# Kernel optimization log

Hardware: AMD Instinct MI355X
Metric: run time of the kernel (lower is better)

## Reference

```python
import jax, jax.numpy as jnp
import numpy as np

T, N, D, R, E = 512, 32, 300, 3, 64
NUM_NODES, VG = 70000, 40000


def setup_inputs() -> dict:
    key = jax.random.key(0)
    ks = jax.random.split(key, 10)
    return {
        "x_indices": jax.random.randint(ks[0], (T, N), 0, NUM_NODES),
        "edge_src": jax.random.randint(ks[1], (T, R, E), 0, N),
        "edge_dst": jax.random.randint(ks[2], (T, R, E), 0, N),
        "X": jax.random.normal(ks[3], (NUM_NODES, D), dtype=jnp.float32) * 0.1,
        "conv_W": jax.random.normal(ks[4], (R, D, D), dtype=jnp.float32) * 0.05,
        "W0": jax.random.normal(ks[5], (D, D), dtype=jnp.float32) * 0.05,
        "Wu": jax.random.normal(ks[6], (N * D, D), dtype=jnp.float32) * 0.01,
        "Uu": jax.random.normal(ks[7], (D, D), dtype=jnp.float32) * 0.05,
        "Wg": jax.random.normal(ks[8], (VG, D), dtype=jnp.float32) * 0.05,
        "bg": jnp.zeros((VG,), dtype=jnp.float32),
    }


def gcn_conv(x, W, src, dst):
    """torch_geometric GCNConv(bias=False): add self-loops, D^-1/2 (A+I) D^-1/2 (x W)."""
    n = x.shape[0]
    h = x @ W  # [N, D]
    loop = jnp.arange(n)
    s = jnp.concatenate([src, loop])
    t = jnp.concatenate([dst, loop])
    deg = jax.ops.segment_sum(jnp.ones_like(t, dtype=x.dtype), t, num_segments=n)
    dinv = jnp.where(deg > 0, jax.lax.rsqrt(jnp.maximum(deg, 1e-12)), 0.0)
    norm = dinv[s] * dinv[t]  # [E+N]
    return jax.ops.segment_sum(h[s] * norm[:, None], t, num_segments=n)


def reference(x_indices, edge_src, edge_dst, X, conv_W, W0, Wu, Uu, Wg, bg):
    def step(mem, inp):
        idx, src, dst = inp  # [N], [R,E], [R,E]
        x = X[idx]  # grapharea features [N, D]
        # sum of per-relation GCNConv outputs
        conv = jnp.sum(
            jax.vmap(gcn_conv, in_axes=(None, 0, 0, 0))(x, conv_W, src, dst), axis=0
        )
        proposed = conv + x @ W0  # eye(N) @ (x @ W0) == x @ W0
        # GRU-style update gate: [1, N*D] @ [N*D, D] + mem_row0 @ [D, D]
        gate = jax.nn.sigmoid(x.reshape(1, -1) @ Wu + mem[0:1] @ Uu)  # [1, D]
        new_mem = gate * proposed + (1.0 - gate) * mem  # broadcast over N rows
        logits = jnp.maximum(new_mem[0], 0.0) @ Wg.T + bg  # [VG]
        # memory is a non-grad buffer in torch (.data.copy_): stop gradient through time
        return jax.lax.stop_gradient(new_mem), jax.nn.log_softmax(logits)

    mem0 = jnp.zeros((N, D), dtype=X.dtype)
    _, log_probs = jax.lax.scan(step, mem0, (x_indices, edge_src, edge_dst))
    # include_senses=False: per-step torch.tensor(0) stacked -> zeros([T])
    return log_probs, jnp.zeros((x_indices.shape[0],), dtype=jnp.int32)
```

## Files before the change

kernel.cpp:

```cpp
#include <hip/hip_runtime.h>
#include <hip/hip_bf16.h>
#include <math.h>

#define T_ 512
#define N_ 32
#define D_ 300
#define R_ 3
#define E_ 64
#define VG_ 40000

typedef __attribute__((ext_vector_type(8))) short bf16x8;
typedef __attribute__((ext_vector_type(4))) float f32x4;

#define LGKM_BARRIER() asm volatile("s_waitcnt lgkmcnt(0)\n\ts_barrier" ::: "memory")

static __device__ inline unsigned short f2b(float f) {
  __hip_bfloat16 h = __float2bfloat16(f);
  return *(unsigned short*)&h;
}

__global__ void k_zero(float* __restrict__ p, int n) {
  int i = blockIdx.x * blockDim.x + threadIdx.x;
  if (i < n) p[i] = 0.f;
}

__global__ void k_tr_wu(const float* __restrict__ Wu, unsigned short* __restrict__ Wt) {
  __shared__ float s[32][33];
  int kb = blockIdx.x * 32, nb = blockIdx.y * 32;
  int tn = threadIdx.x & 31, tr = threadIdx.x >> 5;
  for (int i = tr; i < 32; i += 8) {
    int k = kb + i, n = nb + tn;
    s[i][tn] = (n < 300) ? Wu[(size_t)k * 300 + n] : 0.f;
  }
  __syncthreads();
  for (int i = tr; i < 32; i += 8) {
    int n = nb + i, k = kb + tn;
    Wt[(size_t)n * 9600 + k] = f2b(s[tn][i]);
  }
}

__global__ void k_tr_wcat(const float* __restrict__ convW, const float* __restrict__ W0,
                          unsigned short* __restrict__ Wt) {
  __shared__ float s[32][33];
  int kb = blockIdx.x * 32, nb = blockIdx.y * 32;
  int tn = threadIdx.x & 31, tr = threadIdx.x >> 5;
  for (int i = tr; i < 32; i += 8) {
    int k = kb + i, n = nb + tn;
    float v = 0.f;
    if (n < 300 && k < 1200)
      v = (k < 900) ? convW[(size_t)k * 300 + n] : W0[(size_t)(k - 900) * 300 + n];
    s[i][tn] = v;
  }
  __syncthreads();
  for (int i = tr; i < 32; i += 8) {
    int n = nb + i, k = kb + tn;
    Wt[(size_t)n * 1216 + k] = f2b(s[tn][i]);
  }
}

__global__ void k_gather(const int* __restrict__ xidx, const int* __restrict__ esrc,
                         const int* __restrict__ edst, const float* __restrict__ X,
                         unsigned short* __restrict__ xg, unsigned short* __restrict__ Ag)
{
  const int t = blockIdx.x;
  __shared__ int s_idx[N_];
  __shared__ int s_src[R_][E_];
  __shared__ int s_dst[R_][E_];
  __shared__ int s_deg[R_][N_];
  __shared__ float s_dinv[R_][N_];
  const int tid = threadIdx.x;

  if (tid < N_) s_idx[tid] = xidx[t * N_ + tid];
  if (tid < R_ * E_) {
    int r = tid / E_, e = tid % E_;
    s_src[r][e] = esrc[(t * R_ + r) * E_ + e];
    s_dst[r][e] = edst[(t * R_ + r) * E_ + e];
  }
  if (tid < R_ * N_) ((int*)s_deg)[tid] = 1;
  __syncthreads();
  if (tid < R_ * E_) {
    int r = tid / E_;
    atomicAdd(&s_deg[r][s_dst[r][tid % E_]], 1);
  }
  __syncthreads();
  if (tid < R_ * N_) ((float*)s_dinv)[tid] = rsqrtf((float)((int*)s_deg)[tid]);
  __syncthreads();

  for (int nd = tid; nd < N_ * D_; nd += blockDim.x) {
    int n = nd / D_, d = nd % D_;
    xg[(size_t)t * (N_ * D_) + nd] = f2b(X[(size_t)s_idx[n] * D_ + d]);
  }
  if (tid < D_) {
    int d = tid;
    float x0 = X[(size_t)s_idx[0] * D_ + d];
    #pragma unroll
    for (int r = 0; r < R_; ++r) {
      float dinv0 = s_dinv[r][0];
      float acc = dinv0 * dinv0 * x0;
      for (int e = 0; e < E_; ++e) {
        if (s_dst[r][e] == 0) {
          int s = s_src[r][e];
          acc += s_dinv[r][s] * dinv0 * X[(size_t)s_idx[s] * D_ + d];
        }
      }
      Ag[(size_t)t * 1216 + r * D_ + d] = f2b(acc);
    }
    Ag[(size_t)t * 1216 + 900 + d] = f2b(x0);
  }
  if (tid < 16) Ag[(size_t)t * 1216 + 1200 + tid] = 0;
}

template<bool ATOMIC>
__global__ __launch_bounds__(256) void k_bgemm(
    const unsigned short* __restrict__ A,
    const unsigned short* __restrict__ B,
    float* __restrict__ C, int ldc, int Ncols, int K, int kchunk)
{
  const int tid = threadIdx.x;
  const int wid = tid >> 6, lane = tid & 63;
  const int l16 = lane & 15, lq = lane >> 4;
  const int bm = blockIdx.x * 128 + (wid & 1) * 64;
  const int bn = blockIdx.y * 128 + (wid >> 1) * 64;
  const int k0 = blockIdx.z * kchunk;
  const int nk = kchunk / 32;

  f32x4 acc[4][4] = {};
  const unsigned short* ap[4];
  const unsigned short* bp[4];
  #pragma unroll
  for (int mt = 0; mt < 4; ++mt) ap[mt] = A + (size_t)(bm + mt * 16 + l16) * K + k0 + lq * 8;
  #pragma unroll
  for (int nt = 0; nt < 4; ++nt) bp[nt] = B + (size_t)(bn + nt * 16 + l16) * K + k0 + lq * 8;

  #pragma unroll 2
  for (int c = 0; c < nk; ++c) {
    bf16x8 af[4], bfr[4];
    #pragma unroll
    for (int mt = 0; mt < 4; ++mt) af[mt] = *(const bf16x8*)(ap[mt] + c * 32);
    #pragma unroll
    for (int nt = 0; nt < 4; ++nt) bfr[nt] = *(const bf16x8*)(bp[nt] + c * 32);
    #pragma unroll
    for (int mt = 0; mt < 4; ++mt)
      #pragma unroll
      for (int nt = 0; nt < 4; ++nt)
        acc[mt][nt] = __builtin_amdgcn_mfma_f32_16x16x32_bf16(af[mt], bfr[nt], acc[mt][nt], 0, 0, 0);
  }

  #pragma unroll
  for (int mt = 0; mt < 4; ++mt) {
    #pragma unroll
    for (int r = 0; r < 4; ++r) {
      int row = bm + mt * 16 + lq * 4 + r;
      #pragma unroll
      for (int nt = 0; nt < 4; ++nt) {
        int col = bn + nt * 16 + l16;
        if (col < Ncols) {
          if (ATOMIC) atomicAdd(&C[(size_t)row * ldc + col], acc[mt][nt][r]);
          else        C[(size_t)row * ldc + col] = acc[mt][nt][r];
        }
      }
    }
  }
}

__global__ __launch_bounds__(256, 2) void k_lgemm(
    const unsigned short* __restrict__ A, const float* __restrict__ Wg,
    const float* __restrict__ bg, float* __restrict__ C)
{
  const int tid = threadIdx.x;
  const int wid = tid >> 6, lane = tid & 63;
  const int l16 = lane & 15, lq = lane >> 4;
  const int bn = blockIdx.x * 64;
  const int m0 = wid * 128;

  f32x4 acc[8][4] = {};
  const unsigned short* ap[8];
  const float* bp[4];
  #pragma unroll
  for (int mt = 0; mt < 8; ++mt) ap[mt] = A + (size_t)(m0 + mt * 16 + l16) * 320 + lq * 8;
  #pragma unroll
  for (int nt = 0; nt < 4; ++nt) bp[nt] = Wg + (size_t)(bn + nt * 16 + l16) * 300;

  #pragma unroll
  for (int c = 0; c < 10; ++c) {
    bf16x8 bfr[4];
    if (c < 9) {
      #pragma unroll
      for (int nt = 0; nt < 4; ++nt) {
        f32x4 x = *(const f32x4*)(bp[nt] + c * 32 + lq * 8);
        f32x4 y = *(const f32x4*)(bp[nt] + c * 32 + lq * 8 + 4);
        bf16x8 bv;
        #pragma unroll
        for (int j = 0; j < 4; ++j) { bv[j] = (short)f2b(x[j]); bv[4 + j] = (short)f2b(y[j]); }
        bfr[nt] = bv;
      }
    } else {
      #pragma unroll
      for (int nt = 0; nt < 4; ++nt) {
        bf16x8 bv;
        #pragma unroll
        for (int j = 0; j < 8; ++j) {
          int k = 288 + lq * 8 + j;
          bv[j] = (short)((k < 300) ? f2b(bp[nt][k]) : 0);
        }
        bfr[nt] = bv;
      }
    }
    bf16x8 af[8];
    #pragma unroll
    for (int mt = 0; mt < 8; ++mt) af[mt] = *(const bf16x8*)(ap[mt] + c * 32);
    #pragma unroll
    for (int mt = 0; mt < 8; ++mt)
      #pragma unroll
      for (int nt = 0; nt < 4; ++nt)
        acc[mt][nt] = __builtin_amdgcn_mfma_f32_16x16x32_bf16(af[mt], bfr[nt], acc[mt][nt], 0, 0, 0);
  }

  float bb[4];
  #pragma unroll
  for (int nt = 0; nt < 4; ++nt) bb[nt] = bg[bn + nt * 16 + l16];
  #pragma unroll
  for (int mt = 0; mt < 8; ++mt) {
    #pragma unroll
    for (int r = 0; r < 4; ++r) {
      int row = m0 + mt * 16 + lq * 4 + r;
      #pragma unroll
      for (int nt = 0; nt < 4; ++nt) {
        int col = bn + nt * 16 + l16;
        C[(size_t)row * VG_ + col] = acc[mt][nt][r] + bb[nt];
      }
    }
  }
}

__global__ __launch_bounds__(640) void k_rec(
    const float* __restrict__ gx, const float* __restrict__ P0,
    const float* __restrict__ Uu, unsigned short* __restrict__ Mrelu_bf)
{
  __shared__ __align__(16) unsigned short m_bf[2][320];
  __shared__ unsigned short mr_s[16 * 320];
  const int tid = threadIdx.x;
  const int wid = tid >> 6, lane = tid & 63;
  const int l16 = lane & 15, lq = lane >> 4;
  const int nt0 = wid * 2, nt1 = wid * 2 + 1;

  bf16x8 b0[10], b1[10];
  {
    int n0 = nt0 * 16 + l16, n1 = nt1 * 16 + l16;
    #pragma unroll
    for (int c = 0; c < 10; ++c) {
      bf16x8 v0, v1;
      #pragma unroll
      for (int j = 0; j < 8; ++j) {
        int k = c * 32 + lq * 8 + j;
        float f0 = (k < 300 && n0 < 300) ? Uu[(size_t)k * 300 + n0] : 0.f;
        float f1 = (k < 300 && n1 < 300) ? Uu[(size_t)k * 300 + n1] : 0.f;
        v0[j] = (short)f2b(f0);
        v1[j] = (short)f2b(f1);
      }
      b0[c] = v0; b1[c] = v1;
    }
  }

  const int c0 = wid * 32 + l16;
  const int c1 = c0 + 16;
  const bool gate = (lq == 0);
  float m0 = 0.f, m1 = 0.f;
  float gx0 = 0.f, gx1 = 0.f, p00 = 0.f, p01 = 0.f;
  if (gate) {
    if (c0 < 300) { gx0 = gx[c0]; p00 = P0[c0]; }
    if (c1 < 300) { gx1 = gx[c1]; p01 = P0[c1]; }
  }

  if (tid < 320) { m_bf[0][tid] = 0; m_bf[1][tid] = 0; }
  for (int i = tid; i < 16 * 320; i += 640) mr_s[i] = 0;
  __syncthreads();

  for (int t = 0; t < T_; ++t) {
    const int rb = t & 1, wb = rb ^ 1;
    bf16x8 a[10];
    #pragma unroll
    for (int c = 0; c < 10; ++c)
      a[c] = *(const bf16x8*)(&m_bf[rb][c * 32 + lq * 8]);
    f32x4 A0 = {0.f,0.f,0.f,0.f}, A1 = {0.f,0.f,0.f,0.f};
    f32x4 B0 = {0.f,0.f,0.f,0.f}, B1 = {0.f,0.f,0.f,0.f};
    #pragma unroll
    for (int cc = 0; cc < 5; ++cc) {
      A0 = __builtin_amdgcn_mfma_f32_16x16x32_bf16(a[cc],     b0[cc],     A0, 0, 0, 0);
      A1 = __builtin_amdgcn_mfma_f32_16x16x32_bf16(a[cc],     b1[cc],     A1, 0, 0, 0);
      B0 = __builtin_amdgcn_mfma_f32_16x16x32_bf16(a[cc + 5], b0[cc + 5], B0, 0, 0, 0);
      B1 = __builtin_amdgcn_mfma_f32_16x16x32_bf16(a[cc + 5], b1[cc + 5], B1, 0, 0, 0);
    }
    if (gate) {
      const int slot = (t & 15) * 320;
      if (c0 < 300) {
        float z = A0[0] + B0[0] + gx0;
        float g = __frcp_rn(1.f + __expf(-z));
        m0 = fmaf(g, p00 - m0, m0);
        m_bf[wb][c0] = f2b(m0);
        mr_s[slot + c0] = f2b(fmaxf(m0, 0.f));
      }
      if (c1 < 300) {
        float z = A1[0] + B1[0] + gx1;
        float g = __frcp_rn(1.f + __expf(-z));
        m1 = fmaf(g, p01 - m1, m1);
        m_bf[wb][c1] = f2b(m1);
        mr_s[slot + c1] = f2b(fmaxf(m1, 0.f));
      }
      if (t + 1 < T_) {
        const size_t o = (size_t)(t + 1) * D_;
        if (c0 < 300) { gx0 = gx[o + c0]; p00 = P0[o + c0]; }
        if (c1 < 300) { gx1 = gx[o + c1]; p01 = P0[o + c1]; }
      }
    }
    LGKM_BARRIER();
    if ((t & 7) == 7) {
      const int base = t - 7;
      const unsigned int* src = (const unsigned int*)(mr_s + (base & 15) * 320);
      unsigned int* dst = (unsigned int*)(Mrelu_bf + (size_t)base * 320);
      for (int w = tid; w < 1280; w += 640) dst[w] = src[w];
    }
  }
}

__global__ __launch_bounds__(256) void k_lsm(float* __restrict__ out) {
  const int t = blockIdx.x;
  float* row = out + (size_t)t * VG_;
  const f32x4* row4 = (const f32x4*)row;
  __shared__ float redM[256];
  __shared__ float redS[256];
  const int tid = threadIdx.x;
  float lm = -1e30f, ls = 0.f;
  for (int v = tid; v < VG_ / 4; v += 256) {
    f32x4 z4 = row4[v];
    #pragma unroll
    for (int j = 0; j < 4; ++j) {
      float z = z4[j];
      float m2 = fmaxf(lm, z);
      ls = ls * expf(lm - m2) + expf(z - m2);
      lm = m2;
    }
  }
  redM[tid] = lm; redS[tid] = ls;
  __syncthreads();
  for (int s = 128; s > 0; s >>= 1) {
    if (tid < s) {
      float mA = redM[tid], mB = redM[tid + s];
      float M = fmaxf(mA, mB);
      redS[tid] = redS[tid] * expf(mA - M) + redS[tid + s] * expf(mB - M);
      redM[tid] = M;
    }
    __syncthreads();
  }
  float lse = redM[0] + logf(redS[0]);
  f32x4* row4w = (f32x4*)row;
  for (int v = tid; v < VG_ / 4; v += 256) {
    f32x4 z4 = row4w[v];
    #pragma unroll
    for (int j = 0; j < 4; ++j) z4[j] -= lse;
    row4w[v] = z4;
  }
  if (tid == 0) out[(size_t)T_ * VG_ + t] = 0.0f;
}

extern "C" void kernel_launch(void* const* d_in, const int* in_sizes, int n_in,
                              void* d_out, int out_size, void* d_ws, size_t ws_size,
                              hipStream_t stream) {
  const int*   xidx  = (const int*)d_in[0];
  const int*   esrc  = (const int*)d_in[1];
  const int*   edst  = (const int*)d_in[2];
  const float* X     = (const float*)d_in[3];
  const float* convW = (const float*)d_in[4];
  const float* W0    = (const float*)d_in[5];
  const float* Wu    = (const float*)d_in[6];
  const float* Uu    = (const float*)d_in[7];
  const float* Wg    = (const float*)d_in[8];
  const float* bg    = (const float*)d_in[9];
  float* out = (float*)d_out;

  char* ws = (char*)d_ws;
  float*          gx     = (float*)ws;
  float*          P0     = (float*)(ws + 614400);
  unsigned short* MreluB = (unsigned short*)(ws + 1228800);
  unsigned short* xgB    = (unsigned short*)(ws + 1556480);
  unsigned short* AgB    = (unsigned short*)(ws + 11386880);
  unsigned short* WuT    = (unsigned short*)(ws + 12632064);
  unsigned short* WcatT  = (unsigned short*)(ws + 20004864);

  k_zero<<<(T_ * D_ + 255) / 256, 256, 0, stream>>>(gx, T_ * D_);
  k_tr_wu<<<dim3(300, 12), 256, 0, stream>>>(Wu, WuT);
  k_tr_wcat<<<dim3(38, 12), 256, 0, stream>>>(convW, W0, WcatT);
  k_gather<<<T_, 320, 0, stream>>>(xidx, esrc, edst, X, xgB, AgB);

  k_bgemm<true><<<dim3(4, 3, 10), 256, 0, stream>>>(xgB, WuT, gx, D_, D_, 9600, 960);
  k_bgemm<false><<<dim3(4, 3, 1), 256, 0, stream>>>(AgB, WcatT, P0, D_, D_, 1216, 1216);

  k_rec<<<1, 640, 0, stream>>>(gx, P0, Uu, MreluB);

  k_lgemm<<<dim3(625), 256, 0, stream>>>(MreluB, Wg, bg, out);
  k_lsm<<<T_, 256, 0, stream>>>(out);
}
```

Measured before the change: 885.7 us.

## Shrink recurrent kernel to 4 waves with 5 column tiles each, pre-transpose Uu

The serial recurrence kernel now runs with 256 threads (4 waves) instead of 640, and each wave computes 5 output column tiles per step. This cuts the barrier cost per timestep and the number of waves that must synchronise. Uu is pre-transposed into bf16 by a new kernel that reuses the xg workspace buffer, so each wave loads its B fragments with vector loads. In exchange each wave holds 50 B-fragment registers and issues more MFMAs serially per step, which lengthens the per-step critical path and raises register pressure.

```diff
diff --git a/kernel.cpp b/kernel.cpp
--- a/kernel.cpp
+++ b/kernel.cpp
@@ -55,6 +55,21 @@
   for (int i = tr; i < 32; i += 8) {
     int n = nb + i, k = kb + tn;
     Wt[(size_t)n * 1216 + k] = f2b(s[tn][i]);
+  }
+}
+
+__global__ void k_tr_uu(const float* __restrict__ Uu, unsigned short* __restrict__ UuT) {
+  __shared__ float s[32][33];
+  int kb = blockIdx.x * 32, nb = blockIdx.y * 32;
+  int tn = threadIdx.x & 31, tr = threadIdx.x >> 5;
+  for (int i = tr; i < 32; i += 8) {
+    int k = kb + i, n = nb + tn;
+    s[i][tn] = (k < 300 && n < 300) ? Uu[(size_t)k * 300 + n] : 0.f;
+  }
+  __syncthreads();
+  for (int i = tr; i < 32; i += 8) {
+    int n = nb + i, k = kb + tn;
+    UuT[(size_t)n * 320 + k] = f2b(s[tn][i]);
   }
 }
 
@@ -233,47 +248,37 @@
   }
 }
 
-__global__ __launch_bounds__(640) void k_rec(
+__global__ __launch_bounds__(256, 1) void k_rec(
     const float* __restrict__ gx, const float* __restrict__ P0,
-    const float* __restrict__ Uu, unsigned short* __restrict__ Mrelu_bf)
+    const unsigned short* __restrict__ UuT, unsigned short* __restrict__ Mrelu_bf)
 {
   __shared__ __align__(16) unsigned short m_bf[2][320];
   __shared__ unsigned short mr_s[16 * 320];
   const int tid = threadIdx.x;
   const int wid = tid >> 6, lane = tid & 63;
   const int l16 = lane & 15, lq = lane >> 4;
-  const int nt0 = wid * 2, nt1 = wid * 2 + 1;
-
-  bf16x8 b0[10], b1[10];
-  {
-    int n0 = nt0 * 16 + l16, n1 = nt1 * 16 + l16;
-    #pragma unroll
-    for (int c = 0; c < 10; ++c) {
-      bf16x8 v0, v1;
-      #pragma unroll
-      for (int j = 0; j < 8; ++j) {
-        int k = c * 32 + lq * 8 + j;
-        float f0 = (k < 300 && n0 < 300) ? Uu[(size_t)k * 300 + n0] : 0.f;
-        float f1 = (k < 300 && n1 < 300) ? Uu[(size_t)k * 300 + n1] : 0.f;
-        v0[j] = (short)f2b(f0);
-        v1[j] = (short)f2b(f1);
-      }
-      b0[c] = v0; b1[c] = v1;
-    }
-  }
-
-  const int c0 = wid * 32 + l16;
-  const int c1 = c0 + 16;
-  const bool gate = (lq == 0);
-  float m0 = 0.f, m1 = 0.f;
-  float gx0 = 0.f, gx1 = 0.f, p00 = 0.f, p01 = 0.f;
-  if (gate) {
-    if (c0 < 300) { gx0 = gx[c0]; p00 = P0[c0]; }
-    if (c1 < 300) { gx1 = gx[c1]; p01 = P0[c1]; }
-  }
-
-  if (tid < 320) { m_bf[0][tid] = 0; m_bf[1][tid] = 0; }
-  for (int i = tid; i < 16 * 320; i += 640) mr_s[i] = 0;
+  const int cb = wid * 80;
+
+  bf16x8 bfr[5][10];
+  #pragma unroll
+  for (int nt = 0; nt < 5; ++nt) {
+    const unsigned short* bp = UuT + (size_t)(cb + nt * 16 + l16) * 320 + lq * 8;
+    #pragma unroll
+    for (int c = 0; c < 10; ++c)
+      bfr[nt][c] = *(const bf16x8*)(bp + c * 32);
+  }
+
+  float mreg[5] = {0.f, 0.f, 0.f, 0.f, 0.f};
+  float gxv[5], p0v[5];
+  #pragma unroll
+  for (int nt = 0; nt < 5; ++nt) {
+    int c = cb + nt * 16 + l16;
+    gxv[nt] = (c < 300) ? gx[c] : 0.f;
+    p0v[nt] = (c < 300) ? P0[c] : 0.f;
+  }
+
+  for (int i = tid; i < 320; i += 256) { m_bf[0][i] = 0; m_bf[1][i] = 0; }
+  for (int i = tid; i < 16 * 320; i += 256) mr_s[i] = 0;
   __syncthreads();
 
   for (int t = 0; t < T_; ++t) {
@@ -282,35 +287,39 @@
     #pragma unroll
     for (int c = 0; c < 10; ++c)
       a[c] = *(const bf16x8*)(&m_bf[rb][c * 32 + lq * 8]);
-    f32x4 A0 = {0.f,0.f,0.f,0.f}, A1 = {0.f,0.f,0.f,0.f};
-    f32x4 B0 = {0.f,0.f,0.f,0.f}, B1 = {0.f,0.f,0.f,0.f};
+    f32x4 acc0[5] = {};
+    f32x4 acc1[5] = {};
     #pragma unroll
     for (int cc = 0; cc < 5; ++cc) {
-      A0 = __builtin_amdgcn_mfma_f32_16x16x32_bf16(a[cc],     b0[cc],     A0, 0, 0, 0);
-      A1 = __builtin_amdgcn_mfma_f32_16x16x32_bf16(a[cc],     b1[cc],     A1, 0, 0, 0);
-      B0 = __builtin_amdgcn_mfma_f32_16x16x32_bf16(a[cc + 5], b0[cc + 5], B0, 0, 0, 0);
-      B1 = __builtin_amdgcn_mfma_f32_16x16x32_bf16(a[cc + 5], b1[cc + 5], B1, 0, 0, 0);
-    }
-    if (gate) {
-      const int slot = (t & 15) * 320;
-      if (c0 < 300) {
-        float z = A0[0] + B0[0] + gx0;
-        float g = __frcp_rn(1.f + __expf(-z));
-        m0 = fmaf(g, p00 - m0, m0);
-        m_bf[wb][c0] = f2b(m0);
-        mr_s[slot + c0] = f2b(fmaxf(m0, 0.f));
-      }
-      if (c1 < 300) {
-        float z = A1[0] + B1[0] + gx1;
-        float g = __frcp_rn(1.f + __expf(-z));
-        m1 = fmaf(g, p01 - m1, m1);
-        m_bf[wb][c1] = f2b(m1);
-        mr_s[slot + c1] = f2b(fmaxf(m1, 0.f));
-      }
-      if (t + 1 < T_) {
-        const size_t o = (size_t)(t + 1) * D_;
-        if (c0 < 300) { gx0 = gx[o + c0]; p00 = P0[o + c0]; }
-        if (c1 < 300) { gx1 = gx[o + c1]; p01 = P0[o + c1]; }
+      #pragma unroll
+      for (int nt = 0; nt < 5; ++nt) {
+        acc0[nt] = __builtin_amdgcn_mfma_f32_16x16x32_bf16(a[cc],     bfr[nt][cc],     acc0[nt], 0, 0, 0);
+        acc1[nt] = __builtin_amdgcn_mfma_f32_16x16x32_bf16(a[cc + 5], bfr[nt][cc + 5], acc1[nt], 0, 0, 0);
+      }
+    }
+    #pragma unroll
+    for (int nt = 0; nt < 5; ++nt) {
+      float z = acc0[nt][0] + acc1[nt][0] + gxv[nt];
+      float g = __frcp_rn(1.f + __expf(-z));
+      mreg[nt] = fmaf(g, p0v[nt] - mreg[nt], mreg[nt]);
+    }
+    const int slot = (t & 15) * 320;
+    if (lq == 0) {
+      #pragma unroll
+      for (int nt = 0; nt < 5; ++nt) {
+        int c = cb + nt * 16 + l16;
+        if (c < 300) {
+          m_bf[wb][c] = f2b(mreg[nt]);
+          mr_s[slot + c] = f2b(fmaxf(mreg[nt], 0.f));
+        }
+      }
+    }
+    if (t + 1 < T_) {
+      const size_t o = (size_t)(t + 1) * D_;
+      #pragma unroll
+      for (int nt = 0; nt < 5; ++nt) {
+        int c = cb + nt * 16 + l16;
+        if (c < 300) { gxv[nt] = gx[o + c]; p0v[nt] = P0[o + c]; }
       }
     }
     LGKM_BARRIER();
@@ -318,7 +327,8 @@
       const int base = t - 7;
       const unsigned int* src = (const unsigned int*)(mr_s + (base & 15) * 320);
       unsigned int* dst = (unsigned int*)(Mrelu_bf + (size_t)base * 320);
-      for (int w = tid; w < 1280; w += 640) dst[w] = src[w];
+      #pragma unroll
+      for (int w = 0; w < 5; ++w) dst[tid + w * 256] = src[tid + w * 256];
     }
   }
 }
@@ -386,6 +396,7 @@
   unsigned short* AgB    = (unsigned short*)(ws + 11386880);
   unsigned short* WuT    = (unsigned short*)(ws + 12632064);
   unsigned short* WcatT  = (unsigned short*)(ws + 20004864);
+  unsigned short* UuT    = xgB;
 
   k_zero<<<(T_ * D_ + 255) / 256, 256, 0, stream>>>(gx, T_ * D_);
   k_tr_wu<<<dim3(300, 12), 256, 0, stream>>>(Wu, WuT);
@@ -395,7 +406,8 @@
   k_bgemm<true><<<dim3(4, 3, 10), 256, 0, stream>>>(xgB, WuT, gx, D_, D_, 9600, 960);
   k_bgemm<false><<<dim3(4, 3, 1), 256, 0, stream>>>(AgB, WcatT, P0, D_, D_, 1216, 1216);
 
-  k_rec<<<1, 640, 0, stream>>>(gx, P0, Uu, MreluB);
+  k_tr_uu<<<dim3(10, 10), 256, 0, stream>>>(Uu, UuT);
+  k_rec<<<1, 256, 0, stream>>>(gx, P0, UuT, MreluB);
 
   k_lgemm<<<dim3(625), 256, 0, stream>>>(MreluB, Wg, bg, out);
   k_lsm<<<T_, 256, 0, stream>>>(out);
```

Result: slower. 934.1 us (+5.5%).
